# Performance work log

Measured on AMD Instinct MI355X. Metric: run time of the kernel, lower is better.

The kernel has to match this reference:

```python
import jax, jax.numpy as jnp
import numpy as np

FEAT_STRIDE = 16
SCORE_THRESH = 0.7
DIST_THRESH = 16.0
MAX_OUT = 50
B = 2048
IMG_W = 65536


def setup_inputs() -> dict:
    key = jax.random.key(0)
    k1, k2, k3 = jax.random.split(key, 3)
    fw = IMG_W // FEAT_STRIDE
    pred_cls_logit = jax.random.normal(k1, (B, fw), dtype=jnp.float32)
    pred_delta = jax.random.normal(k2, (B, fw, 2), dtype=jnp.float32)
    # realistic image widths in [0.5, 1.0] * img_width
    real_images_width = jax.random.uniform(k3, (B,), jnp.float32, 0.5, 1.0) * IMG_W
    return {
        "pred_cls_logit": pred_cls_logit,
        "pred_delta": pred_delta,
        "img_width": IMG_W,
        "real_images_width": real_images_width,
    }


def _nms_one(positions, scores):
    # positions: [N, 2], scores: [N]. Greedy 1D NMS, fixed MAX_OUT iterations.
    centers = positions.mean(axis=1)                      # [N]
    alive0 = scores >= SCORE_THRESH                       # score-threshold filter

    def step(alive, _):
        masked = jnp.where(alive, scores, -1e30)
        i = jnp.argmax(masked)                            # highest remaining score
        has = jnp.any(alive)
        f = has.astype(jnp.float32)                       # 1.0 if a box was picked
        p = positions[i] * f
        s = scores[i] * f
        # suppress everything within DIST_THRESH of picked center (incl. itself)
        new_alive = alive & (jnp.abs(centers - centers[i]) > DIST_THRESH)
        return new_alive, (p, s, f)

    _, (P, S, F) = jax.lax.scan(step, alive0, None, length=MAX_OUT)
    # pad_to_fixed_size: append validity flag column, zero-padded rows
    nms_positions = jnp.concatenate([P, F[:, None]], axis=1)   # [MAX_OUT, 3]
    nms_scores = jnp.concatenate([S[:, None], F[:, None]], axis=1)  # [MAX_OUT, 2]
    return nms_positions, nms_scores


def reference(pred_cls_logit, pred_delta, img_width, real_images_width):
    feat_width = img_width // FEAT_STRIDE
    interval_center = (jnp.arange(feat_width, dtype=jnp.float32) + 0.5) * FEAT_STRIDE
    # [B, feat_width, 2]
    pos = pred_delta * FEAT_STRIDE + interval_center[None, :, None]
    scores = jax.nn.sigmoid(pred_cls_logit)               # [B, feat_width]
    max_width = real_images_width[:, None, None] - 1.0
    pos = jnp.where(pos < 0.0, 0.0, pos)
    pos = jnp.where(pos > max_width, max_width, pos)

    nms_positions, nms_scores = jax.vmap(_nms_one)(pos, scores)

    nms_center = nms_positions[..., :2].mean(axis=2)      # [B, MAX_OUT]
    x_interval_num = jnp.floor(nms_center / FEAT_STRIDE).astype(jnp.int32)
    valid = nms_positions[..., 2] == 1.0
    idx = jnp.where(valid, x_interval_num, feat_width)    # out-of-range -> dropped
    cls_ids = jax.vmap(
        lambda ii: jnp.zeros((feat_width,), jnp.float32).at[ii].set(1.0, mode='drop')
    )(idx)                                                # [B, feat_width]
    return nms_positions, nms_scores, cls_ids
```

## Files before the change

kernel.cpp:

```cpp
#include <hip/hip_runtime.h>
#include <math.h>

#define MAX_OUT 50
#define MAXC 992
#define NJ 16

__device__ __forceinline__ unsigned long long umax64(unsigned long long a,
                                                     unsigned long long b) {
  return a > b ? a : b;
}

__global__ __launch_bounds__(64) void essp_kernel(
    const float* __restrict__ logits,
    const float* __restrict__ deltas,
    const float* __restrict__ realw,
    float* __restrict__ out_pos,
    float* __restrict__ out_scr,
    float* __restrict__ out_cls,
    int fw)
{
  __shared__ unsigned long long c_tmp[MAXC];
  __shared__ float2 c_pp[MAXC];
  __shared__ unsigned long long pk[MAX_OUT];

  const int b = blockIdx.x;
  const int lane = threadIdx.x;
  const float mw = realw[b] - 1.0f;
  const float* lg = logits + (size_t)b * fw;
  const float* dl = deltas + (size_t)b * fw * 2;
  float* cls = out_cls + (size_t)b * fw;

  int cnt = 0;
  for (int base = 0; base < fw; base += 256) {
    const int i0 = base + 4 * lane;
    const float4 lx  = *(const float4*)(lg + i0);
    const float4 d01 = *(const float4*)(dl + 2 * i0);
    const float4 d23 = *(const float4*)(dl + 2 * i0 + 4);
    *(float4*)(cls + i0) = make_float4(0.f, 0.f, 0.f, 0.f);
    const float xs[4] = {lx.x, lx.y, lx.z, lx.w};
    const float dx[4] = {d01.x, d01.z, d23.x, d23.z};
    const float dy[4] = {d01.y, d01.w, d23.y, d23.w};
    #pragma unroll
    for (int e = 0; e < 4; ++e) {
      const int i = i0 + e;
      const float x = xs[e];
      const bool cand = (x >= 0.846f);
      const unsigned long long mask = __ballot(cand);
      if (cand) {
        const int slot = cnt + __popcll(mask & ((1ULL << lane) - 1ULL));
        if (slot < MAXC) {
          const float ic = ((float)i + 0.5f) * 16.0f;
          float p0 = dx[e] * 16.0f + ic;
          float p1 = dy[e] * 16.0f + ic;
          p0 = (p0 < 0.f) ? 0.f : p0;  p0 = (p0 > mw) ? mw : p0;
          p1 = (p1 < 0.f) ? 0.f : p1;  p1 = (p1 > mw) ? mw : p1;
          c_tmp[slot] = ((unsigned long long)__float_as_uint(x) << 32)
                        | (unsigned)i;
          c_pp[slot] = make_float2(p0, p1);
        }
      }
      cnt += __popcll(mask);
    }
  }
  const int n = (cnt < MAXC) ? cnt : MAXC;
  __syncthreads();

  unsigned long long key[NJ];
  float cen[NJ];
  #pragma unroll
  for (int j = 0; j < NJ; ++j) { key[j] = 0ULL; cen[j] = 0.f; }
  #pragma unroll 1
  for (int j = 0; j < NJ; ++j) {
    const int k = lane + 64 * j;
    if (k < n) {
      const unsigned long long t = c_tmp[k];
      const float x = __uint_as_float((unsigned)(t >> 32));
      const unsigned idx = (unsigned)t & 4095u;
      const float s = (float)(1.0 / (1.0 + exp(-(double)x)));
      if (s >= 0.7f) {
        key[j] = ((unsigned long long)__float_as_uint(s) << 22)
               | ((unsigned long long)(idx ^ 4095u) << 10)
               | (unsigned long long)k;
      }
      const float2 pp = c_pp[k];
      cen[j] = (pp.x + pp.y) * 0.5f;
    }
  }
  __syncthreads();

  int npick = MAX_OUT;
  #pragma unroll 1
  for (int it = 0; it < MAX_OUT; ++it) {
    unsigned long long b0 = umax64(umax64(umax64(key[0], key[1]),
                                          umax64(key[2], key[3])),
                                   umax64(umax64(key[4], key[5]),
                                          umax64(key[6], key[7])));
    unsigned long long b1 = umax64(umax64(umax64(key[8],  key[9]),
                                          umax64(key[10], key[11])),
                                   umax64(umax64(key[12], key[13]),
                                          umax64(key[14], key[15])));
    unsigned long long best = umax64(b0, b1);
    #pragma unroll
    for (int off = 1; off < 64; off <<= 1) {
      const unsigned long long o = __shfl_xor(best, off, 64);
      if (o > best) best = o;
    }
    if (best == 0ULL) { npick = it; break; }
    const int bk = (int)(best & 1023ULL);
    const float2 bpp = c_pp[bk];
    const float wc = (bpp.x + bpp.y) * 0.5f;
    if (lane == 0) pk[it] = best;
    #pragma unroll
    for (int j = 0; j < NJ; ++j) {
      if (fabsf(cen[j] - wc) <= 16.0f) key[j] = 0ULL;
    }
  }
  __syncthreads();

  asm volatile("s_waitcnt vmcnt(0)" ::: "memory");
  float* prow = out_pos + (size_t)b * MAX_OUT * 3;
  float* srow = out_scr + (size_t)b * MAX_OUT * 2;
  if (lane < MAX_OUT) {
    if (lane < npick) {
      const unsigned long long k2 = pk[lane];
      const int slot = (int)(k2 & 1023ULL);
      const float2 pp = c_pp[slot];
      const float s = __uint_as_float((unsigned)(k2 >> 22));
      prow[lane * 3 + 0] = pp.x;
      prow[lane * 3 + 1] = pp.y;
      prow[lane * 3 + 2] = 1.0f;
      srow[lane * 2 + 0] = s;
      srow[lane * 2 + 1] = 1.0f;
      const float wc = (pp.x + pp.y) * 0.5f;
      const int ci = (int)floorf(wc * 0.0625f);
      if (ci >= 0 && ci < fw) cls[ci] = 1.0f;
    } else {
      prow[lane * 3 + 0] = 0.0f;
      prow[lane * 3 + 1] = 0.0f;
      prow[lane * 3 + 2] = 0.0f;
      srow[lane * 2 + 0] = 0.0f;
      srow[lane * 2 + 1] = 0.0f;
    }
  }
}

extern "C" void kernel_launch(void* const* d_in, const int* in_sizes, int n_in,
                              void* d_out, int out_size, void* d_ws, size_t ws_size,
                              hipStream_t stream) {
  const float* logits = (const float*)d_in[0];
  const float* deltas = (const float*)d_in[1];
  const float* realw  = (const float*)d_in[3];
  const int Bn = in_sizes[3];
  const int fw = in_sizes[0] / Bn;
  float* out_pos = (float*)d_out;
  float* out_scr = out_pos + (size_t)Bn * MAX_OUT * 3;
  float* out_cls = out_scr + (size_t)Bn * MAX_OUT * 2;
  essp_kernel<<<Bn, 64, 0, stream>>>(logits, deltas, realw,
                                     out_pos, out_scr, out_cls, fw);
}
```

Baseline: 66.48 us.

## Split row streaming across four waves with segmented candidate buffers and float-score NMS

```diff
diff --git a/kernel.cpp b/kernel.cpp
--- a/kernel.cpp
+++ b/kernel.cpp
@@ -2,15 +2,12 @@
 #include <math.h>
 
 #define MAX_OUT 50
-#define MAXC 992
-#define NJ 16
+#define SEGCAP 288
+#define NWAVES 4
+#define MAXC (SEGCAP * NWAVES)
+#define NJ 18
 
-__device__ __forceinline__ unsigned long long umax64(unsigned long long a,
-                                                     unsigned long long b) {
-  return a > b ? a : b;
-}
-
-__global__ __launch_bounds__(64) void essp_kernel(
+__global__ __launch_bounds__(256) void essp_kernel(
     const float* __restrict__ logits,
     const float* __restrict__ deltas,
     const float* __restrict__ realw,
@@ -19,120 +16,117 @@
     float* __restrict__ out_cls,
     int fw)
 {
-  __shared__ unsigned long long c_tmp[MAXC];
+  __shared__ float  c_s[MAXC];
+  __shared__ float  c_cen[MAXC];
   __shared__ float2 c_pp[MAXC];
-  __shared__ unsigned long long pk[MAX_OUT];
+  __shared__ int    pk[MAX_OUT];
 
-  const int b = blockIdx.x;
-  const int lane = threadIdx.x;
+  const int b    = blockIdx.x;
+  const int tid  = threadIdx.x;
+  const int lane = tid & 63;
+  const int w    = tid >> 6;
+
   const float mw = realw[b] - 1.0f;
-  const float* lg = logits + (size_t)b * fw;
-  const float* dl = deltas + (size_t)b * fw * 2;
+  const float*  lg  = logits + (size_t)b * fw;
+  const float2* dl2 = (const float2*)(deltas + (size_t)b * fw * 2);
   float* cls = out_cls + (size_t)b * fw;
 
+  const int segbase = w * SEGCAP;
+  #pragma unroll
+  for (int j = 0; j < 5; ++j) {
+    const int k = lane + 64 * j;
+    if (k < SEGCAP) { c_s[segbase + k] = -1e30f; c_cen[segbase + k] = 0.0f; }
+  }
+
+  const int ebase = w * 1024;
   int cnt = 0;
-  for (int base = 0; base < fw; base += 256) {
-    const int i0 = base + 4 * lane;
-    const float4 lx  = *(const float4*)(lg + i0);
-    const float4 d01 = *(const float4*)(dl + 2 * i0);
-    const float4 d23 = *(const float4*)(dl + 2 * i0 + 4);
-    *(float4*)(cls + i0) = make_float4(0.f, 0.f, 0.f, 0.f);
-    const float xs[4] = {lx.x, lx.y, lx.z, lx.w};
-    const float dx[4] = {d01.x, d01.z, d23.x, d23.z};
-    const float dy[4] = {d01.y, d01.w, d23.y, d23.w};
-    #pragma unroll
-    for (int e = 0; e < 4; ++e) {
-      const int i = i0 + e;
-      const float x = xs[e];
-      const bool cand = (x >= 0.846f);
-      const unsigned long long mask = __ballot(cand);
-      if (cand) {
-        const int slot = cnt + __popcll(mask & ((1ULL << lane) - 1ULL));
-        if (slot < MAXC) {
-          const float ic = ((float)i + 0.5f) * 16.0f;
-          float p0 = dx[e] * 16.0f + ic;
-          float p1 = dy[e] * 16.0f + ic;
-          p0 = (p0 < 0.f) ? 0.f : p0;  p0 = (p0 > mw) ? mw : p0;
-          p1 = (p1 < 0.f) ? 0.f : p1;  p1 = (p1 > mw) ? mw : p1;
-          c_tmp[slot] = ((unsigned long long)__float_as_uint(x) << 32)
-                        | (unsigned)i;
-          c_pp[slot] = make_float2(p0, p1);
-        }
+  #pragma unroll 4
+  for (int r = 0; r < 16; ++r) {
+    const int i = ebase + r * 64 + lane;
+    const float  x = lg[i];
+    const float2 d = dl2[i];
+    cls[i] = 0.0f;
+    const bool cand = (x >= 0.846f);
+    const unsigned long long mask = __ballot(cand);
+    if (cand) {
+      const int slot = cnt + __popcll(mask & ((1ULL << lane) - 1ULL));
+      if (slot < SEGCAP) {
+        const float ic = ((float)i + 0.5f) * 16.0f;
+        float p0 = d.x * 16.0f + ic;
+        float p1 = d.y * 16.0f + ic;
+        p0 = (p0 < 0.f) ? 0.f : p0;  p0 = (p0 > mw) ? mw : p0;
+        p1 = (p1 < 0.f) ? 0.f : p1;  p1 = (p1 > mw) ? mw : p1;
+        const int gs = segbase + slot;
+        c_s[gs]   = x;
+        c_cen[gs] = (p0 + p1) * 0.5f;
+        c_pp[gs]  = make_float2(p0, p1);
       }
-      cnt += __popcll(mask);
+    }
+    cnt += __popcll(mask);
+  }
+
+  const int nc = (cnt < SEGCAP) ? cnt : SEGCAP;
+  #pragma unroll 1
+  for (int j = 0; j < 5; ++j) {
+    const int k = lane + 64 * j;
+    if (k < nc) {
+      const float x = c_s[segbase + k];
+      const float s = (float)(1.0 / (1.0 + exp(-(double)x)));
+      c_s[segbase + k] = (s >= 0.7f) ? s : -1e30f;
     }
   }
-  const int n = (cnt < MAXC) ? cnt : MAXC;
+
   __syncthreads();
+  if (w != 0) return;
 
-  unsigned long long key[NJ];
-  float cen[NJ];
+  float sv[NJ], cv[NJ];
   #pragma unroll
-  for (int j = 0; j < NJ; ++j) { key[j] = 0ULL; cen[j] = 0.f; }
-  #pragma unroll 1
   for (int j = 0; j < NJ; ++j) {
-    const int k = lane + 64 * j;
-    if (k < n) {
-      const unsigned long long t = c_tmp[k];
-      const float x = __uint_as_float((unsigned)(t >> 32));
-      const unsigned idx = (unsigned)t & 4095u;
-      const float s = (float)(1.0 / (1.0 + exp(-(double)x)));
-      if (s >= 0.7f) {
-        key[j] = ((unsigned long long)__float_as_uint(s) << 22)
-               | ((unsigned long long)(idx ^ 4095u) << 10)
-               | (unsigned long long)k;
-      }
-      const float2 pp = c_pp[k];
-      cen[j] = (pp.x + pp.y) * 0.5f;
-    }
+    sv[j] = c_s[lane + 64 * j];
+    cv[j] = c_cen[lane + 64 * j];
   }
-  __syncthreads();
+  if (lane < MAX_OUT) pk[lane] = -1;
 
-  int npick = MAX_OUT;
   #pragma unroll 1
   for (int it = 0; it < MAX_OUT; ++it) {
-    unsigned long long b0 = umax64(umax64(umax64(key[0], key[1]),
-                                          umax64(key[2], key[3])),
-                                   umax64(umax64(key[4], key[5]),
-                                          umax64(key[6], key[7])));
-    unsigned long long b1 = umax64(umax64(umax64(key[8],  key[9]),
-                                          umax64(key[10], key[11])),
-                                   umax64(umax64(key[12], key[13]),
-                                          umax64(key[14], key[15])));
-    unsigned long long best = umax64(b0, b1);
+    float best = fmaxf(sv[0], sv[1]);
+    #pragma unroll
+    for (int j = 2; j < NJ; ++j) best = fmaxf(best, sv[j]);
+    #pragma unroll
+    for (int off = 1; off < 64; off <<= 1)
+      best = fmaxf(best, __shfl_xor(best, off, 64));
+    if (best < 0.7f) break;
+
+    int jsel = 127;
+    #pragma unroll
+    for (int j = NJ - 1; j >= 0; --j) if (sv[j] == best) jsel = j;
+    int slotv = (jsel << 6) | lane;
     #pragma unroll
     for (int off = 1; off < 64; off <<= 1) {
-      const unsigned long long o = __shfl_xor(best, off, 64);
-      if (o > best) best = o;
+      const int o = __shfl_xor(slotv, off, 64);
+      slotv = (o < slotv) ? o : slotv;
     }
-    if (best == 0ULL) { npick = it; break; }
-    const int bk = (int)(best & 1023ULL);
-    const float2 bpp = c_pp[bk];
-    const float wc = (bpp.x + bpp.y) * 0.5f;
-    if (lane == 0) pk[it] = best;
+
+    const float wc = c_cen[slotv];
+    if (lane == 0) pk[it] = slotv;
     #pragma unroll
-    for (int j = 0; j < NJ; ++j) {
-      if (fabsf(cen[j] - wc) <= 16.0f) key[j] = 0ULL;
-    }
+    for (int j = 0; j < NJ; ++j)
+      if (fabsf(cv[j] - wc) <= 16.0f) sv[j] = -1e30f;
   }
-  __syncthreads();
 
-  asm volatile("s_waitcnt vmcnt(0)" ::: "memory");
   float* prow = out_pos + (size_t)b * MAX_OUT * 3;
   float* srow = out_scr + (size_t)b * MAX_OUT * 2;
   if (lane < MAX_OUT) {
-    if (lane < npick) {
-      const unsigned long long k2 = pk[lane];
-      const int slot = (int)(k2 & 1023ULL);
+    const int slot = pk[lane];
+    if (slot >= 0) {
       const float2 pp = c_pp[slot];
-      const float s = __uint_as_float((unsigned)(k2 >> 22));
       prow[lane * 3 + 0] = pp.x;
       prow[lane * 3 + 1] = pp.y;
       prow[lane * 3 + 2] = 1.0f;
-      srow[lane * 2 + 0] = s;
+      srow[lane * 2 + 0] = c_s[slot];
       srow[lane * 2 + 1] = 1.0f;
-      const float wc = (pp.x + pp.y) * 0.5f;
-      const int ci = (int)floorf(wc * 0.0625f);
+      const float wcc = c_cen[slot];
+      const int ci = (int)floorf(wcc * 0.0625f);
       if (ci >= 0 && ci < fw) cls[ci] = 1.0f;
     } else {
       prow[lane * 3 + 0] = 0.0f;
@@ -155,6 +149,6 @@
   float* out_pos = (float*)d_out;
   float* out_scr = out_pos + (size_t)Bn * MAX_OUT * 3;
   float* out_cls = out_scr + (size_t)Bn * MAX_OUT * 2;
-  essp_kernel<<<Bn, 64, 0, stream>>>(logits, deltas, realw,
-                                     out_pos, out_scr, out_cls, fw);
+  essp_kernel<<<Bn, 256, 0, stream>>>(logits, deltas, realw,
+                                      out_pos, out_scr, out_cls, fw);
 }
```

Result: slower. 74.19 us (+11.6%).
